# Kernel tuning notes

Hardware: AMD Instinct MI355X
Metric: run time of the kernel (lower is better)

Reference implementation:

```python
import jax, jax.numpy as jnp
import numpy as np

N = 50000      # nodes
E = 800000     # edges (avg degree 16)
F_IN = 64      # node_features (== GENConv out, so no input projection)
H = 64         # hidden
EXP = 2 * H    # GENConv MLP expansion dim = 128
D2 = F_IN + H  # dense-block concat dim = SAGEConv in = 128
EPS_MSG = 1e-7 # GENConv message eps
BN_EPS = 1e-5


def setup_inputs() -> dict:
    key = jax.random.key(0)
    ks = jax.random.split(key, 16)
    g = lambda k, shape, fan: jax.random.normal(k, shape, jnp.float32) / np.sqrt(fan)
    return {
        "x": jax.random.normal(ks[0], (N, F_IN), jnp.float32),
        "edge_index": jax.random.randint(ks[1], (2, E), 0, N, jnp.int32),
        # GENConv MLP: Linear(64,128) -> BatchNorm(128) -> ReLU -> Linear(128,64)
        "W1": g(ks[2], (H, EXP), H), "b1": jnp.zeros((EXP,), jnp.float32),
        "gamma": jnp.ones((EXP,), jnp.float32), "beta": jnp.zeros((EXP,), jnp.float32),
        "W2": g(ks[3], (EXP, H), EXP), "b2": jnp.zeros((H,), jnp.float32),
        # SAGEConv project Linear(128,128), lin_l Linear(128,64), lin_r Linear(128,64,bias=False)
        "Wp": g(ks[4], (D2, D2), D2), "bp": jnp.zeros((D2,), jnp.float32),
        "Wl": g(ks[5], (D2, H), D2), "bl": jnp.zeros((H,), jnp.float32),
        "Wr": g(ks[6], (D2, H), D2),
        # fc Linear(64,1)
        "Wf": g(ks[7], (H, 1), H), "bf": jnp.zeros((1,), jnp.float32),
    }


def _forward(x, W1, b1, gamma, beta, W2, b2, Wp, bp, Wl, bl, Wr, Wf, bf, src, dst):
    n = x.shape[0]
    # ---- GENConv(aggr='softmax', t=1.0): msg = relu(x_j) + eps -------------
    msg = jax.nn.relu(x[src]) + EPS_MSG                       # [E, H]
    mmax = jax.ops.segment_max(msg, dst, num_segments=n)      # per-dst, per-feature max
    mmax = jax.lax.stop_gradient(jnp.where(jnp.isfinite(mmax), mmax, 0.0))
    e = jnp.exp(msg - mmax[dst])                              # t = 1.0
    denom = jax.ops.segment_sum(e, dst, num_segments=n)
    numer = jax.ops.segment_sum(e * msg, dst, num_segments=n)
    agg = numer / jnp.where(denom > 0, denom, 1.0)            # softmax aggregation
    out = agg + x                                             # residual with x_dst
    # GENConv MLP (BatchNorm in training mode: batch stats, biased var)
    h = out @ W1 + b1
    mu = h.mean(axis=0)
    var = h.var(axis=0)
    h = (h - mu) * jax.lax.rsqrt(var + BN_EPS) * gamma + beta
    h = jax.nn.relu(h) @ W2 + b2                              # [N, H]
    # ---- DeepGCNLayer block='dense': concat input ---------------------------
    x2 = jnp.concatenate([x, h], axis=-1)                     # [N, F_IN+H]
    x2 = jax.nn.sigmoid(x2)                                   # self.relu = Sigmoid()
    # ---- SAGEConv(project=True, aggr=DeepSetsAggregation()==sum) -----------
    xp = jax.nn.relu(x2 @ Wp + bp)                            # projected source feats
    aggr = jax.ops.segment_sum(xp[src], dst, num_segments=n)  # DeepSets w/o nns = sum
    out2 = aggr @ Wl + bl + x2 @ Wr                           # root uses UNprojected x2
    out2 = jax.nn.sigmoid(out2)
    logits = out2 @ Wf + bf                                   # [N, 1]
    probs = jax.nn.sigmoid(logits)                            # training branch
    return probs, logits


def reference(x, edge_index, W1, b1, gamma, beta, W2, b2, Wp, bp, Wl, bl, Wr, Wf, bf):
    src, dst = edge_index[0], edge_index[1]
    return _forward(x, W1, b1, gamma, beta, W2, b2, Wp, bp, Wl, bl, Wr, Wf, bf, src, dst)
```

## Files before the change

kernel.cpp:

```cpp
#include <hip/hip_runtime.h>

#define F_IN 64
#define HID 64
#define EXPD 128
#define D2 128
#define MAXDEG 64
#define NBW 128
#define NB 391
#define BINCAP 2400
#define EPT 32

typedef __attribute__((ext_vector_type(8))) short bf16x8;
typedef __attribute__((ext_vector_type(4))) float f32x4;

__device__ __forceinline__ float sigmoidf_(float x) {
    return 1.0f / (1.0f + __expf(-x));
}
__device__ __forceinline__ unsigned bf16rne_(float f) {
    unsigned u = __float_as_uint(f);
    return (u + 0x7FFFu + ((u >> 16) & 1u)) >> 16;
}
__device__ __forceinline__ float bf16tof_(unsigned u16) {
    return __uint_as_float(u16 << 16);
}

__global__ __launch_bounds__(256) void k_bin(const int* __restrict__ ei,
                                             int* __restrict__ binCount,
                                             unsigned* __restrict__ binned,
                                             const float* __restrict__ x,
                                             unsigned short* __restrict__ x16,
                                             const float* __restrict__ W1,
                                             const float* __restrict__ W2,
                                             const float* __restrict__ Wp,
                                             const float* __restrict__ Wl,
                                             const float* __restrict__ Wr,
                                             short* __restrict__ dst,
                                             int nE, int n, int nbinb) {
    int b = blockIdx.x;
    if (b < nbinb) {
        __shared__ int hist[NB];
        __shared__ int base[NB];
        int tid = threadIdx.x;
        for (int i = tid; i < NB; i += 256) hist[i] = 0;
        __syncthreads();
        unsigned ed[EPT];
        unsigned short rk[EPT];
        int e0 = b * (256 * EPT);
#pragma unroll
        for (int j = 0; j < EPT; ++j) {
            int e = e0 + j * 256 + tid;
            if (e < nE) {
                unsigned s = (unsigned)ei[e];
                unsigned d = (unsigned)ei[nE + e];
                ed[j] = s | (d << 16);
                rk[j] = (unsigned short)atomicAdd(&hist[d >> 7], 1);
            }
        }
        __syncthreads();
        for (int i = tid; i < NB; i += 256) {
            int h = hist[i];
            base[i] = h > 0 ? atomicAdd(&binCount[i], h) : 0;
        }
        __syncthreads();
#pragma unroll
        for (int j = 0; j < EPT; ++j) {
            int e = e0 + j * 256 + tid;
            if (e < nE) {
                int bin = (ed[j] >> 16) >> 7;
                int pos = base[bin] + (int)rk[j];
                if (pos < BINCAP) binned[(size_t)bin * BINCAP + pos] = ed[j];
            }
        }
        return;
    }
    b -= nbinb;
    if (b < 192) {
        int e = b * 256 + threadIdx.x;
        const float* src;
        int K, N, base2;
        if (e < 8192)       { src = W1; K = 64;  N = 128; base2 = 0; }
        else if (e < 16384) { src = W2; K = 128; N = 64;  base2 = 8192; }
        else if (e < 32768) { src = Wp; K = 128; N = 128; base2 = 16384; }
        else if (e < 40960) { src = Wl; K = 128; N = 64;  base2 = 32768; }
        else                { src = Wr; K = 128; N = 64;  base2 = 40960; }
        int le = e - base2;
        int j = le & 7;
        int lane = (le >> 3) & 63;
        int n16 = lane & 15, q = lane >> 4;
        int rest = le >> 9;
        int KC = K / 32;
        int kc = rest % KC, nt = rest / KC;
        int k = kc * 32 + q * 8 + j;
        int col = nt * 16 + n16;
        dst[e] = (short)bf16rne_(src[(size_t)k * N + col]);
        return;
    }
    int i0 = (b - 192) * 1024 + threadIdx.x * 4;
    if (i0 < n * F_IN) {
        float4 v = *(const float4*)(x + i0);
        uint2 pk;
        pk.x = bf16rne_(v.x) | (bf16rne_(v.y) << 16);
        pk.y = bf16rne_(v.z) | (bf16rne_(v.w) << 16);
        *(uint2*)(x16 + i0) = pk;
    }
}

__global__ __launch_bounds__(256) void k_csr(const int* __restrict__ binCount,
                                             const unsigned* __restrict__ binned,
                                             int* __restrict__ counts,
                                             unsigned short* __restrict__ csr, int n) {
    __shared__ unsigned short lcsr[NBW * MAXDEG];
    __shared__ int lcnt[NBW];
    int b = blockIdx.x;
    int tid = threadIdx.x;
    if (tid < NBW) lcnt[tid] = 0;
    __syncthreads();
    int cnt = binCount[b];
    cnt = cnt < BINCAP ? cnt : BINCAP;
    const unsigned* src = binned + (size_t)b * BINCAP;
    for (int i = tid; i < cnt; i += 256) {
        unsigned u = src[i];
        int dl = (int)(u >> 16) - b * NBW;
        int slot = atomicAdd(&lcnt[dl], 1);
        if (slot < MAXDEG) lcsr[dl * MAXDEG + slot] = (unsigned short)(u & 0xFFFF);
    }
    __syncthreads();
    int nodebase = b * NBW;
    if (tid < NBW && nodebase + tid < n) counts[nodebase + tid] = lcnt[tid];
    int nrows = n - nodebase;
    nrows = nrows < NBW ? nrows : NBW;
    int nu4 = nrows * 8;
    uint4* dstrow = (uint4*)(csr + (size_t)nodebase * MAXDEG);
    for (int idx = tid; idx < nu4; idx += 256) dstrow[idx] = ((const uint4*)lcsr)[idx];
}

__global__ __launch_bounds__(256) void k_gen(const unsigned short* __restrict__ x16,
                                             const int* __restrict__ counts,
                                             const unsigned short* __restrict__ csr,
                                             unsigned short* __restrict__ gen16, int n) {
    const unsigned* x32 = (const unsigned*)x16;
    int wid = threadIdx.x >> 6;
    int lane = threadIdx.x & 63;
    int H = lane >> 5, f2 = lane & 31;
    int v = blockIdx.x * 4 + wid;
    if (v >= n) return;
    int deg = counts[v];
    deg = deg > MAXDEG ? MAXDEG : deg;
    int idx = 0;
    if (lane < deg) idx = (int)csr[(size_t)v * MAXDEG + lane];
    float d0 = 0.f, d1 = 0.f, n0 = 0.f, n1 = 0.f;
    int i = 0;
    for (; i + 8 <= deg; i += 8) {
        int sA = __shfl(idx, i + 0 + H, 64);
        int sB = __shfl(idx, i + 2 + H, 64);
        int sC = __shfl(idx, i + 4 + H, 64);
        int sD = __shfl(idx, i + 6 + H, 64);
        unsigned uA = x32[(size_t)sA * 32 + f2];
        unsigned uB = x32[(size_t)sB * 32 + f2];
        unsigned uC = x32[(size_t)sC * 32 + f2];
        unsigned uD = x32[(size_t)sD * 32 + f2];
#pragma unroll
        for (int t = 0; t < 4; ++t) {
            unsigned u = t == 0 ? uA : t == 1 ? uB : t == 2 ? uC : uD;
            float m0 = fmaxf(bf16tof_(u & 0xFFFF), 0.f) + 1e-7f;
            float m1 = fmaxf(bf16tof_(u >> 16), 0.f) + 1e-7f;
            float e0 = __expf(m0), e1 = __expf(m1);
            d0 += e0; d1 += e1;
            n0 = fmaf(e0, m0, n0);
            n1 = fmaf(e1, m1, n1);
        }
    }
    for (; i + 2 <= deg; i += 2) {
        int s = __shfl(idx, i + H, 64);
        unsigned u = x32[(size_t)s * 32 + f2];
        float m0 = fmaxf(bf16tof_(u & 0xFFFF), 0.f) + 1e-7f;
        float m1 = fmaxf(bf16tof_(u >> 16), 0.f) + 1e-7f;
        float e0 = __expf(m0), e1 = __expf(m1);
        d0 += e0; d1 += e1;
        n0 = fmaf(e0, m0, n0);
        n1 = fmaf(e1, m1, n1);
    }
    if (i < deg) {
        int s = __shfl(idx, i, 64);
        if (H == 0) {
            unsigned u = x32[(size_t)s * 32 + f2];
            float m0 = fmaxf(bf16tof_(u & 0xFFFF), 0.f) + 1e-7f;
            float m1 = fmaxf(bf16tof_(u >> 16), 0.f) + 1e-7f;
            float e0 = __expf(m0), e1 = __expf(m1);
            d0 += e0; d1 += e1;
            n0 = fmaf(e0, m0, n0);
            n1 = fmaf(e1, m1, n1);
        }
    }
    d0 += __shfl_xor(d0, 32, 64);
    d1 += __shfl_xor(d1, 32, 64);
    n0 += __shfl_xor(n0, 32, 64);
    n1 += __shfl_xor(n1, 32, 64);
    if (H == 0) {
        float a0 = (deg > 0) ? (n0 / d0) : 0.f;
        float a1 = (deg > 0) ? (n1 / d1) : 0.f;
        unsigned xv = x32[(size_t)v * 32 + f2];
        float r0 = a0 + bf16tof_(xv & 0xFFFF);
        float r1 = a1 + bf16tof_(xv >> 16);
        ((unsigned*)gen16)[(size_t)v * 32 + f2] =
            bf16rne_(r0) | (bf16rne_(r1) << 16);
    }
}

__global__ __launch_bounds__(256) void k_gemm1(const unsigned short* __restrict__ gen16,
                                               const short* __restrict__ Wf,
                                               const float* __restrict__ b1,
                                               unsigned short* __restrict__ h16,
                                               float* __restrict__ bnsums, int n) {
    __shared__ short As[64 * 64];
    __shared__ float bnred[256];
    int tid = threadIdx.x;
    int rblk = blockIdx.x * 64;
    if (tid < 256) bnred[tid] = 0.f;
#pragma unroll
    for (int it = 0; it < 2; ++it) {
        int c = it * 256 + tid;
        int rr = c & 63, q8 = c >> 6;
        int gr = rblk + rr;
        gr = gr < n ? gr : n - 1;
        uint4 v = *(const uint4*)(gen16 + (size_t)gr * F_IN + q8 * 8);
        int slot = ((rr >> 4) * 2 + (q8 >> 2)) * 64 + (q8 & 3) * 16 + (rr & 15);
        *(uint4*)(As + slot * 8) = v;
    }
    __syncthreads();
    int L = tid & 63, w = tid >> 6;
    int q = L >> 4, n16 = L & 15;
    int mt_base = (w & 1) * 2;
    int nt_base = (w >> 1) * 4;
    f32x4 acc[2][4];
#pragma unroll
    for (int mt = 0; mt < 2; ++mt)
#pragma unroll
        for (int nt = 0; nt < 4; ++nt) acc[mt][nt] = (f32x4){0.f, 0.f, 0.f, 0.f};
#pragma unroll
    for (int kc = 0; kc < 2; ++kc) {
        bf16x8 a0 = *(const bf16x8*)(As + (((mt_base + 0) * 2 + kc) * 64 + L) * 8);
        bf16x8 a1 = *(const bf16x8*)(As + (((mt_base + 1) * 2 + kc) * 64 + L) * 8);
#pragma unroll
        for (int nt = 0; nt < 4; ++nt) {
            bf16x8 b = *(const bf16x8*)(Wf + (size_t)(((nt_base + nt) * 2 + kc) * 64 + L) * 8);
            acc[0][nt] = __builtin_amdgcn_mfma_f32_16x16x32_bf16(a0, b, acc[0][nt], 0, 0, 0);
            acc[1][nt] = __builtin_amdgcn_mfma_f32_16x16x32_bf16(a1, b, acc[1][nt], 0, 0, 0);
        }
    }
#pragma unroll
    for (int nt = 0; nt < 4; ++nt) {
        int col = (nt_base + nt) * 16 + n16;
        float bv = b1[col];
        float s = 0.f, s2 = 0.f;
#pragma unroll
        for (int mt = 0; mt < 2; ++mt)
#pragma unroll
            for (int r = 0; r < 4; ++r) {
                int row = rblk + (w & 1) * 32 + mt * 16 + q * 4 + r;
                float hv = acc[mt][nt][r] + bv;
                if (row < n) {
                    h16[(size_t)row * EXPD + col] = (unsigned short)bf16rne_(hv);
                    s += hv;
                    s2 = fmaf(hv, hv, s2);
                }
            }
        s += __shfl_xor(s, 16, 64);
        s += __shfl_xor(s, 32, 64);
        s2 += __shfl_xor(s2, 16, 64);
        s2 += __shfl_xor(s2, 32, 64);
        if (q == 0) {
            atomicAdd(&bnred[col], s);
            atomicAdd(&bnred[128 + col], s2);
        }
    }
    __syncthreads();
    if (tid < 256) atomicAdd(&bnsums[tid], bnred[tid]);
}

__global__ __launch_bounds__(256) void k_mlp2a(const unsigned short* __restrict__ h16,
                                               const float* __restrict__ bnsums,
                                               const float* __restrict__ gamma,
                                               const float* __restrict__ beta,
                                               const short* __restrict__ Wf,
                                               const float* __restrict__ b2,
                                               const unsigned short* __restrict__ x16,
                                               unsigned short* __restrict__ x2_16,
                                               float inv_n, int n) {
    __shared__ short As[128 * 128];
    __shared__ float ssl[256];
    int tid = threadIdx.x;
    int rblk = blockIdx.x * 128;
    if (tid < 128) {
        float mu = bnsums[tid] * inv_n;
        float var = fmaf(-mu, mu, bnsums[128 + tid] * inv_n);
        float rs = rsqrtf(fmaxf(var, 0.f) + 1e-5f);
        float scale = gamma[tid] * rs;
        ssl[tid] = scale;
        ssl[128 + tid] = fmaf(-mu, scale, beta[tid]);
    }
    __syncthreads();
#pragma unroll
    for (int it = 0; it < 8; ++it) {
        int c = it * 256 + tid;
        int rr = c & 127, q8 = c >> 7;
        int gr = rblk + rr;
        gr = gr < n ? gr : n - 1;
        uint4 v = *(const uint4*)(h16 + (size_t)gr * EXPD + q8 * 8);
        float4 sc1 = *(const float4*)(ssl + q8 * 8);
        float4 sc2 = *(const float4*)(ssl + q8 * 8 + 4);
        float4 sh1 = *(const float4*)(ssl + 128 + q8 * 8);
        float4 sh2 = *(const float4*)(ssl + 128 + q8 * 8 + 4);
        float o0 = fmaxf(fmaf(bf16tof_(v.x & 0xFFFF), sc1.x, sh1.x), 0.f);
        float o1 = fmaxf(fmaf(bf16tof_(v.x >> 16),    sc1.y, sh1.y), 0.f);
        float o2 = fmaxf(fmaf(bf16tof_(v.y & 0xFFFF), sc1.z, sh1.z), 0.f);
        float o3 = fmaxf(fmaf(bf16tof_(v.y >> 16),    sc1.w, sh1.w), 0.f);
        float o4 = fmaxf(fmaf(bf16tof_(v.z & 0xFFFF), sc2.x, sh2.x), 0.f);
        float o5 = fmaxf(fmaf(bf16tof_(v.z >> 16),    sc2.y, sh2.y), 0.f);
        float o6 = fmaxf(fmaf(bf16tof_(v.w & 0xFFFF), sc2.z, sh2.z), 0.f);
        float o7 = fmaxf(fmaf(bf16tof_(v.w >> 16),    sc2.w, sh2.w), 0.f);
        uint4 pk;
        pk.x = bf16rne_(o0) | (bf16rne_(o1) << 16);
        pk.y = bf16rne_(o2) | (bf16rne_(o3) << 16);
        pk.z = bf16rne_(o4) | (bf16rne_(o5) << 16);
        pk.w = bf16rne_(o6) | (bf16rne_(o7) << 16);
        int slot = ((rr >> 4) * 4 + (q8 >> 2)) * 64 + (q8 & 3) * 16 + (rr & 15);
        *(uint4*)(As + slot * 8) = pk;
    }
    __syncthreads();
    int L = tid & 63, w = tid >> 6;
    int q = L >> 4, n16 = L & 15;
    int mt_base = w * 2;
    f32x4 acc[2][4];
#pragma unroll
    for (int mt = 0; mt < 2; ++mt)
#pragma unroll
        for (int nt = 0; nt < 4; ++nt) acc[mt][nt] = (f32x4){0.f, 0.f, 0.f, 0.f};
#pragma unroll
    for (int kc = 0; kc < 4; ++kc) {
        bf16x8 a0 = *(const bf16x8*)(As + (((mt_base + 0) * 4 + kc) * 64 + L) * 8);
        bf16x8 a1 = *(const bf16x8*)(As + (((mt_base + 1) * 4 + kc) * 64 + L) * 8);
#pragma unroll
        for (int nt = 0; nt < 4; ++nt) {
            bf16x8 b = *(const bf16x8*)(Wf + (size_t)((nt * 4 + kc) * 64 + L) * 8);
            acc[0][nt] = __builtin_amdgcn_mfma_f32_16x16x32_bf16(a0, b, acc[0][nt], 0, 0, 0);
            acc[1][nt] = __builtin_amdgcn_mfma_f32_16x16x32_bf16(a1, b, acc[1][nt], 0, 0, 0);
        }
    }
#pragma unroll
    for (int it = 0; it < 8; ++it) {
        int i = it * 256 + tid;
        int rr = i >> 4, c4 = i & 15;
        int row = rblk + rr;
        if (row < n) {
            uint2 xv = ((const uint2*)x16)[(size_t)row * 16 + c4];
            float s0 = sigmoidf_(bf16tof_(xv.x & 0xFFFF));
            float s1 = sigmoidf_(bf16tof_(xv.x >> 16));
            float s2 = sigmoidf_(bf16tof_(xv.y & 0xFFFF));
            float s3 = sigmoidf_(bf16tof_(xv.y >> 16));
            uint2 pk;
            pk.x = bf16rne_(s0) | (bf16rne_(s1) << 16);
            pk.y = bf16rne_(s2) | (bf16rne_(s3) << 16);
            *(uint2*)(x2_16 + (size_t)row * D2 + c4 * 4) = pk;
        }
    }
#pragma unroll
    for (int nt = 0; nt < 4; ++nt) {
        int col = nt * 16 + n16;
        float bv = b2[col];
#pragma unroll
        for (int mt = 0; mt < 2; ++mt)
#pragma unroll
            for (int r = 0; r < 4; ++r) {
                int row = rblk + w * 32 + mt * 16 + q * 4 + r;
                if (row < n)
                    x2_16[(size_t)row * D2 + 64 + col] =
                        (unsigned short)bf16rne_(sigmoidf_(acc[mt][nt][r] + bv));
            }
    }
}

__global__ __launch_bounds__(256) void k_mlp2b(const unsigned short* __restrict__ x2_16,
                                               const short* __restrict__ Wfp,
                                               const short* __restrict__ Wfl,
                                               const short* __restrict__ Wfr,
                                               const float* __restrict__ bp,
                                               unsigned short* __restrict__ yp16,
                                               unsigned short* __restrict__ yr16, int n) {
    __shared__ short As[64 * 128];
    int tid = threadIdx.x;
    int rblk = blockIdx.x * 64;
#pragma unroll
    for (int it = 0; it < 4; ++it) {
        int c = it * 256 + tid;
        int rr = c & 63, q8 = c >> 6;
        int gr = rblk + rr;
        gr = gr < n ? gr : n - 1;
        uint4 v = *(const uint4*)(x2_16 + (size_t)gr * D2 + q8 * 8);
        int slot = ((rr >> 4) * 4 + (q8 >> 2)) * 64 + (q8 & 3) * 16 + (rr & 15);
        *(uint4*)(As + slot * 8) = v;
    }
    __syncthreads();
    int L = tid & 63, w = tid >> 6;
    int q = L >> 4, n16 = L & 15;
    int mt_base = (w & 1) * 2;
    int nt_base = (w >> 1) * 4;
    f32x4 acc[2][4];
    f32x4 accr[2][2];
#pragma unroll
    for (int mt = 0; mt < 2; ++mt) {
#pragma unroll
        for (int nt = 0; nt < 4; ++nt) acc[mt][nt] = (f32x4){0.f, 0.f, 0.f, 0.f};
#pragma unroll
        for (int nt = 0; nt < 2; ++nt) accr[mt][nt] = (f32x4){0.f, 0.f, 0.f, 0.f};
    }
#pragma unroll
    for (int kc = 0; kc < 4; ++kc) {
        bf16x8 a0 = *(const bf16x8*)(As + (((mt_base + 0) * 4 + kc) * 64 + L) * 8);
        bf16x8 a1 = *(const bf16x8*)(As + (((mt_base + 1) * 4 + kc) * 64 + L) * 8);
#pragma unroll
        for (int nt = 0; nt < 4; ++nt) {
            bf16x8 b = *(const bf16x8*)(Wfp + (size_t)(((nt_base + nt) * 4 + kc) * 64 + L) * 8);
            acc[0][nt] = __builtin_amdgcn_mfma_f32_16x16x32_bf16(a0, b, acc[0][nt], 0, 0, 0);
            acc[1][nt] = __builtin_amdgcn_mfma_f32_16x16x32_bf16(a1, b, acc[1][nt], 0, 0, 0);
        }
#pragma unroll
        for (int nt = 0; nt < 2; ++nt) {
            bf16x8 b = *(const bf16x8*)(Wfr + (size_t)((((w >> 1) * 2 + nt) * 4 + kc) * 64 + L) * 8);
            accr[0][nt] = __builtin_amdgcn_mfma_f32_16x16x32_bf16(a0, b, accr[0][nt], 0, 0, 0);
            accr[1][nt] = __builtin_amdgcn_mfma_f32_16x16x32_bf16(a1, b, accr[1][nt], 0, 0, 0);
        }
    }
#pragma unroll
    for (int nt = 0; nt < 2; ++nt) {
        int col = ((w >> 1) * 2 + nt) * 16 + n16;
#pragma unroll
        for (int mt = 0; mt < 2; ++mt)
#pragma unroll
            for (int r = 0; r < 4; ++r) {
                int row = rblk + (w & 1) * 32 + mt * 16 + q * 4 + r;
                if (row < n)
                    yr16[(size_t)row * HID + col] = (unsigned short)bf16rne_(accr[mt][nt][r]);
            }
    }
    __syncthreads();
#pragma unroll
    for (int nt = 0; nt < 4; ++nt) {
        int kk = (nt_base + nt) * 16 + n16;
        float bv = bp[kk];
        int q8b = kk >> 3, jb = kk & 7;
#pragma unroll
        for (int mt = 0; mt < 2; ++mt)
#pragma unroll
            for (int r = 0; r < 4; ++r) {
                int rr2 = (w & 1) * 32 + mt * 16 + q * 4 + r;
                float xv = fmaxf(acc[mt][nt][r] + bv, 0.f);
                int slot = ((rr2 >> 4) * 4 + (q8b >> 2)) * 64 + (q8b & 3) * 16 + (rr2 & 15);
                As[slot * 8 + jb] = (short)bf16rne_(xv);
            }
    }
    __syncthreads();
    f32x4 acc2[4];
#pragma unroll
    for (int nt = 0; nt < 4; ++nt) acc2[nt] = (f32x4){0.f, 0.f, 0.f, 0.f};
#pragma unroll
    for (int kc = 0; kc < 4; ++kc) {
        bf16x8 a = *(const bf16x8*)(As + ((w * 4 + kc) * 64 + L) * 8);
#pragma unroll
        for (int nt = 0; nt < 4; ++nt) {
            bf16x8 b = *(const bf16x8*)(Wfl + (size_t)((nt * 4 + kc) * 64 + L) * 8);
            acc2[nt] = __builtin_amdgcn_mfma_f32_16x16x32_bf16(a, b, acc2[nt], 0, 0, 0);
        }
    }
#pragma unroll
    for (int nt = 0; nt < 4; ++nt) {
        int col = nt * 16 + n16;
#pragma unroll
        for (int r = 0; r < 4; ++r) {
            int row = rblk + w * 16 + q * 4 + r;
            if (row < n)
                yp16[(size_t)row * HID + col] = (unsigned short)bf16rne_(acc2[nt][r]);
        }
    }
}

__global__ __launch_bounds__(256) void k_sagef(const unsigned short* __restrict__ yp16,
                                               const int* __restrict__ counts,
                                               const unsigned short* __restrict__ csr,
                                               const unsigned short* __restrict__ yr16,
                                               const float* __restrict__ bl,
                                               const float* __restrict__ Wfv,
                                               const float* __restrict__ bf,
                                               float* __restrict__ out, int n) {
    const unsigned* yp32 = (const unsigned*)yp16;
    int wid = threadIdx.x >> 6;
    int lane = threadIdx.x & 63;
    int H = lane >> 5, f2 = lane & 31;
    int v = blockIdx.x * 4 + wid;
    if (v >= n) return;
    int deg = counts[v];
    deg = deg > MAXDEG ? MAXDEG : deg;
    int idx = 0;
    if (lane < deg) idx = (int)csr[(size_t)v * MAXDEG + lane];
    float a0 = 0.f, a1 = 0.f;
    int i = 0;
    for (; i + 8 <= deg; i += 8) {
        int sA = __shfl(idx, i + 0 + H, 64);
        int sB = __shfl(idx, i + 2 + H, 64);
        int sC = __shfl(idx, i + 4 + H, 64);
        int sD = __shfl(idx, i + 6 + H, 64);
        unsigned uA = yp32[(size_t)sA * 32 + f2];
        unsigned uB = yp32[(size_t)sB * 32 + f2];
        unsigned uC = yp32[(size_t)sC * 32 + f2];
        unsigned uD = yp32[(size_t)sD * 32 + f2];
        a0 += bf16tof_(uA & 0xFFFF) + bf16tof_(uB & 0xFFFF) +
              bf16tof_(uC & 0xFFFF) + bf16tof_(uD & 0xFFFF);
        a1 += bf16tof_(uA >> 16) + bf16tof_(uB >> 16) +
              bf16tof_(uC >> 16) + bf16tof_(uD >> 16);
    }
    for (; i + 2 <= deg; i += 2) {
        int s = __shfl(idx, i + H, 64);
        unsigned u = yp32[(size_t)s * 32 + f2];
        a0 += bf16tof_(u & 0xFFFF);
        a1 += bf16tof_(u >> 16);
    }
    if (i < deg) {
        int s = __shfl(idx, i, 64);
        if (H == 0) {
            unsigned u = yp32[(size_t)s * 32 + f2];
            a0 += bf16tof_(u & 0xFFFF);
            a1 += bf16tof_(u >> 16);
        }
    }
    a0 += __shfl_xor(a0, 32, 64);
    a1 += __shfl_xor(a1, 32, 64);
    if (H == 0) {
        unsigned u = ((const unsigned*)yr16)[(size_t)v * 32 + f2];
        float2 blv = ((const float2*)bl)[f2];
        float2 wv  = ((const float2*)Wfv)[f2];
        float o0 = sigmoidf_(a0 + blv.x + bf16tof_(u & 0xFFFF));
        float o1 = sigmoidf_(a1 + blv.y + bf16tof_(u >> 16));
        float t = fmaf(o0, wv.x, o1 * wv.y);
        t += __shfl_xor(t, 1, 64);
        t += __shfl_xor(t, 2, 64);
        t += __shfl_xor(t, 4, 64);
        t += __shfl_xor(t, 8, 64);
        t += __shfl_xor(t, 16, 64);
        if (f2 == 0) {
            float lg = t + bf[0];
            out[v] = sigmoidf_(lg);
            out[n + v] = lg;
        }
    }
}

extern "C" void kernel_launch(void* const* d_in, const int* in_sizes, int n_in,
                              void* d_out, int out_size, void* d_ws, size_t ws_size,
                              hipStream_t stream) {
    const float* x     = (const float*)d_in[0];
    const int*   ei    = (const int*)d_in[1];
    const float* W1    = (const float*)d_in[2];
    const float* b1    = (const float*)d_in[3];
    const float* gamma = (const float*)d_in[4];
    const float* beta  = (const float*)d_in[5];
    const float* W2    = (const float*)d_in[6];
    const float* b2    = (const float*)d_in[7];
    const float* Wp    = (const float*)d_in[8];
    const float* bp    = (const float*)d_in[9];
    const float* Wl    = (const float*)d_in[10];
    const float* bl    = (const float*)d_in[11];
    const float* Wr    = (const float*)d_in[12];
    const float* Wfv   = (const float*)d_in[13];
    const float* bf    = (const float*)d_in[14];
    const int n = in_sizes[0] / F_IN;
    const int e = in_sizes[1] / 2;

    char* ws = (char*)d_ws;
    size_t off = 0;
    auto alloc = [&](size_t bytes) -> void* {
        void* p = (void*)(ws + off);
        off += (bytes + 255) & ~(size_t)255;
        return p;
    };
    float*          bnsums   = (float*)alloc(256 * 4 + NB * 4);
    int*            binCount = (int*)((char*)bnsums + 1024);
    int*            counts   = (int*)alloc((size_t)n * 4);
    unsigned short* csr      = (unsigned short*)alloc((size_t)n * MAXDEG * 2);
    unsigned*       binned   = (unsigned*)alloc((size_t)NB * BINCAP * 4);
    unsigned short* x16      = (unsigned short*)alloc((size_t)n * F_IN * 2);
    unsigned short* gen16    = (unsigned short*)alloc((size_t)n * F_IN * 2);
    unsigned short* h16      = (unsigned short*)alloc((size_t)n * EXPD * 2);
    unsigned short* x2_16    = (unsigned short*)alloc((size_t)n * D2 * 2);
    unsigned short* yp16     = (unsigned short*)alloc((size_t)n * HID * 2);
    unsigned short* yr16     = (unsigned short*)alloc((size_t)n * HID * 2);
    short*          wfrag    = (short*)alloc(49152 * 2);

    float* out = (float*)d_out;
    const int nb64  = (n + 63) / 64;
    const int nb128 = (n + 127) / 128;
    const int nb4   = (n + 3) / 4;
    const int nbinb = (e + 256 * EPT - 1) / (256 * EPT);
    const int nfp = nbinb + 192 + ((n * F_IN + 1023) / 1024);

    hipMemsetAsync(bnsums, 0, 1024 + NB * 4, stream);

    k_bin<<<nfp, 256, 0, stream>>>(ei, binCount, binned, x, x16, W1, W2, Wp, Wl,
                                   Wr, wfrag, e, n, nbinb);
    k_csr<<<NB, 256, 0, stream>>>(binCount, binned, counts, csr, n);
    k_gen<<<nb4, 256, 0, stream>>>(x16, counts, csr, gen16, n);
    k_gemm1<<<nb64, 256, 0, stream>>>(gen16, wfrag, b1, h16, bnsums, n);
    k_mlp2a<<<nb128, 256, 0, stream>>>(h16, bnsums, gamma, beta, wfrag + 8192, b2,
                                       x16, x2_16, 1.0f / (float)n, n);
    k_mlp2b<<<nb64, 256, 0, stream>>>(x2_16, wfrag + 16384, wfrag + 32768,
                                      wfrag + 40960, bp, yp16, yr16, n);
    k_sagef<<<nb4, 256, 0, stream>>>(yp16, counts, csr, yr16, bl, Wfv, bf, out, n);
}
```

Before: 228.9 us.

## Fuse softmax aggregation into GEMM1, merge MLP kernels, drop global bin atomics

The GENConv softmax gather now runs inside the first GEMM kernel and writes its result straight to shared memory, so the gen16 intermediate disappears. The two MLP kernels are merged so the x2 concat/sigmoid tile stays on-chip instead of passing through global memory. Edge binning now uses per-block sub-bins with fixed capacity instead of global atomics, and the memset is folded into k_bin. Costs: 64-row blocks with serial per-wave gathers give fewer waves for latency hiding, and a per-block sub-bin cap of 64 could drop edges on skewed inputs.

```diff
diff --git a/kernel.cpp b/kernel.cpp
--- a/kernel.cpp
+++ b/kernel.cpp
@@ -7,7 +7,8 @@
 #define MAXDEG 64
 #define NBW 128
 #define NB 391
-#define BINCAP 2400
+#define NBINB 98
+#define SUBCAP 64
 #define EPT 32
 
 typedef __attribute__((ext_vector_type(8))) short bf16x8;
@@ -25,8 +26,8 @@
 }
 
 __global__ __launch_bounds__(256) void k_bin(const int* __restrict__ ei,
-                                             int* __restrict__ binCount,
-                                             unsigned* __restrict__ binned,
+                                             int* __restrict__ cnt2,
+                                             unsigned* __restrict__ binned2,
                                              const float* __restrict__ x,
                                              unsigned short* __restrict__ x16,
                                              const float* __restrict__ W1,
@@ -35,12 +36,13 @@
                                              const float* __restrict__ Wl,
                                              const float* __restrict__ Wr,
                                              short* __restrict__ dst,
+                                             float* __restrict__ bnsums,
                                              int nE, int n, int nbinb) {
     int b = blockIdx.x;
+    int tid = threadIdx.x;
     if (b < nbinb) {
         __shared__ int hist[NB];
-        __shared__ int base[NB];
-        int tid = threadIdx.x;
+        if (b == 0) bnsums[tid] = 0.f;
         for (int i = tid; i < NB; i += 256) hist[i] = 0;
         __syncthreads();
         unsigned ed[EPT];
@@ -57,25 +59,22 @@
             }
         }
         __syncthreads();
-        for (int i = tid; i < NB; i += 256) {
-            int h = hist[i];
-            base[i] = h > 0 ? atomicAdd(&binCount[i], h) : 0;
-        }
-        __syncthreads();
+        for (int i = tid; i < NB; i += 256) cnt2[b * NB + i] = hist[i];
 #pragma unroll
         for (int j = 0; j < EPT; ++j) {
             int e = e0 + j * 256 + tid;
             if (e < nE) {
                 int bin = (ed[j] >> 16) >> 7;
-                int pos = base[bin] + (int)rk[j];
-                if (pos < BINCAP) binned[(size_t)bin * BINCAP + pos] = ed[j];
+                int r = (int)rk[j];
+                if (r < SUBCAP)
+                    binned2[((size_t)bin * nbinb + b) * SUBCAP + r] = ed[j];
             }
         }
         return;
     }
     b -= nbinb;
     if (b < 192) {
-        int e = b * 256 + threadIdx.x;
+        int e = b * 256 + tid;
         const float* src;
         int K, N, base2;
         if (e < 8192)       { src = W1; K = 64;  N = 128; base2 = 0; }
@@ -95,7 +94,7 @@
         dst[e] = (short)bf16rne_(src[(size_t)k * N + col]);
         return;
     }
-    int i0 = (b - 192) * 1024 + threadIdx.x * 4;
+    int i0 = (b - 192) * 1024 + tid * 4;
     if (i0 < n * F_IN) {
         float4 v = *(const float4*)(x + i0);
         uint2 pk;
@@ -105,24 +104,33 @@
     }
 }
 
-__global__ __launch_bounds__(256) void k_csr(const int* __restrict__ binCount,
-                                             const unsigned* __restrict__ binned,
+__global__ __launch_bounds__(256) void k_csr(const int* __restrict__ cnt2,
+                                             const unsigned* __restrict__ binned2,
                                              int* __restrict__ counts,
-                                             unsigned short* __restrict__ csr, int n) {
+                                             unsigned short* __restrict__ csr,
+                                             int n, int nbinb) {
     __shared__ unsigned short lcsr[NBW * MAXDEG];
     __shared__ int lcnt[NBW];
+    __shared__ int scnt[NBINB];
     int b = blockIdx.x;
     int tid = threadIdx.x;
     if (tid < NBW) lcnt[tid] = 0;
-    __syncthreads();
-    int cnt = binCount[b];
-    cnt = cnt < BINCAP ? cnt : BINCAP;
-    const unsigned* src = binned + (size_t)b * BINCAP;
-    for (int i = tid; i < cnt; i += 256) {
-        unsigned u = src[i];
-        int dl = (int)(u >> 16) - b * NBW;
-        int slot = atomicAdd(&lcnt[dl], 1);
-        if (slot < MAXDEG) lcsr[dl * MAXDEG + slot] = (unsigned short)(u & 0xFFFF);
+    for (int i = tid; i < nbinb; i += 256) {
+        int c = cnt2[i * NB + b];
+        scnt[i] = c < SUBCAP ? c : SUBCAP;
+    }
+    __syncthreads();
+    const unsigned* src = binned2 + (size_t)b * nbinb * SUBCAP;
+    int tot = nbinb * SUBCAP;
+    for (int i = tid; i < tot; i += 256) {
+        int blk = i >> 6;
+        int r = i & (SUBCAP - 1);
+        if (r < scnt[blk]) {
+            unsigned u = src[i];
+            int dl = (int)(u >> 16) - b * NBW;
+            int slot = atomicAdd(&lcnt[dl], 1);
+            if (slot < MAXDEG) lcsr[dl * MAXDEG + slot] = (unsigned short)(u & 0xFFFF);
+        }
     }
     __syncthreads();
     int nodebase = b * NBW;
@@ -134,101 +142,95 @@
     for (int idx = tid; idx < nu4; idx += 256) dstrow[idx] = ((const uint4*)lcsr)[idx];
 }
 
-__global__ __launch_bounds__(256) void k_gen(const unsigned short* __restrict__ x16,
-                                             const int* __restrict__ counts,
-                                             const unsigned short* __restrict__ csr,
-                                             unsigned short* __restrict__ gen16, int n) {
-    const unsigned* x32 = (const unsigned*)x16;
-    int wid = threadIdx.x >> 6;
-    int lane = threadIdx.x & 63;
-    int H = lane >> 5, f2 = lane & 31;
-    int v = blockIdx.x * 4 + wid;
-    if (v >= n) return;
-    int deg = counts[v];
-    deg = deg > MAXDEG ? MAXDEG : deg;
-    int idx = 0;
-    if (lane < deg) idx = (int)csr[(size_t)v * MAXDEG + lane];
-    float d0 = 0.f, d1 = 0.f, n0 = 0.f, n1 = 0.f;
-    int i = 0;
-    for (; i + 8 <= deg; i += 8) {
-        int sA = __shfl(idx, i + 0 + H, 64);
-        int sB = __shfl(idx, i + 2 + H, 64);
-        int sC = __shfl(idx, i + 4 + H, 64);
-        int sD = __shfl(idx, i + 6 + H, 64);
-        unsigned uA = x32[(size_t)sA * 32 + f2];
-        unsigned uB = x32[(size_t)sB * 32 + f2];
-        unsigned uC = x32[(size_t)sC * 32 + f2];
-        unsigned uD = x32[(size_t)sD * 32 + f2];
-#pragma unroll
-        for (int t = 0; t < 4; ++t) {
-            unsigned u = t == 0 ? uA : t == 1 ? uB : t == 2 ? uC : uD;
-            float m0 = fmaxf(bf16tof_(u & 0xFFFF), 0.f) + 1e-7f;
-            float m1 = fmaxf(bf16tof_(u >> 16), 0.f) + 1e-7f;
-            float e0 = __expf(m0), e1 = __expf(m1);
-            d0 += e0; d1 += e1;
-            n0 = fmaf(e0, m0, n0);
-            n1 = fmaf(e1, m1, n1);
-        }
-    }
-    for (; i + 2 <= deg; i += 2) {
-        int s = __shfl(idx, i + H, 64);
-        unsigned u = x32[(size_t)s * 32 + f2];
-        float m0 = fmaxf(bf16tof_(u & 0xFFFF), 0.f) + 1e-7f;
-        float m1 = fmaxf(bf16tof_(u >> 16), 0.f) + 1e-7f;
-        float e0 = __expf(m0), e1 = __expf(m1);
-        d0 += e0; d1 += e1;
-        n0 = fmaf(e0, m0, n0);
-        n1 = fmaf(e1, m1, n1);
-    }
-    if (i < deg) {
-        int s = __shfl(idx, i, 64);
-        if (H == 0) {
-            unsigned u = x32[(size_t)s * 32 + f2];
-            float m0 = fmaxf(bf16tof_(u & 0xFFFF), 0.f) + 1e-7f;
-            float m1 = fmaxf(bf16tof_(u >> 16), 0.f) + 1e-7f;
-            float e0 = __expf(m0), e1 = __expf(m1);
-            d0 += e0; d1 += e1;
-            n0 = fmaf(e0, m0, n0);
-            n1 = fmaf(e1, m1, n1);
-        }
-    }
-    d0 += __shfl_xor(d0, 32, 64);
-    d1 += __shfl_xor(d1, 32, 64);
-    n0 += __shfl_xor(n0, 32, 64);
-    n1 += __shfl_xor(n1, 32, 64);
-    if (H == 0) {
-        float a0 = (deg > 0) ? (n0 / d0) : 0.f;
-        float a1 = (deg > 0) ? (n1 / d1) : 0.f;
-        unsigned xv = x32[(size_t)v * 32 + f2];
-        float r0 = a0 + bf16tof_(xv & 0xFFFF);
-        float r1 = a1 + bf16tof_(xv >> 16);
-        ((unsigned*)gen16)[(size_t)v * 32 + f2] =
-            bf16rne_(r0) | (bf16rne_(r1) << 16);
-    }
-}
-
-__global__ __launch_bounds__(256) void k_gemm1(const unsigned short* __restrict__ gen16,
-                                               const short* __restrict__ Wf,
-                                               const float* __restrict__ b1,
-                                               unsigned short* __restrict__ h16,
-                                               float* __restrict__ bnsums, int n) {
+__global__ __launch_bounds__(256) void k_geng(const unsigned short* __restrict__ x16,
+                                              const int* __restrict__ counts,
+                                              const unsigned short* __restrict__ csr,
+                                              const short* __restrict__ Wf,
+                                              const float* __restrict__ b1,
+                                              unsigned short* __restrict__ h16,
+                                              float* __restrict__ bnsums, int n) {
     __shared__ short As[64 * 64];
     __shared__ float bnred[256];
+    const unsigned* x32 = (const unsigned*)x16;
     int tid = threadIdx.x;
+    int w = tid >> 6;
+    int lane = tid & 63;
+    int H = lane >> 5, f2 = lane & 31;
     int rblk = blockIdx.x * 64;
-    if (tid < 256) bnred[tid] = 0.f;
-#pragma unroll
-    for (int it = 0; it < 2; ++it) {
-        int c = it * 256 + tid;
-        int rr = c & 63, q8 = c >> 6;
-        int gr = rblk + rr;
-        gr = gr < n ? gr : n - 1;
-        uint4 v = *(const uint4*)(gen16 + (size_t)gr * F_IN + q8 * 8);
+    bnred[tid] = 0.f;
+    for (int t = 0; t < 16; ++t) {
+        int rr = w * 16 + t;
+        int v = rblk + rr;
+        int q8 = f2 >> 2;
         int slot = ((rr >> 4) * 2 + (q8 >> 2)) * 64 + (q8 & 3) * 16 + (rr & 15);
-        *(uint4*)(As + slot * 8) = v;
-    }
-    __syncthreads();
-    int L = tid & 63, w = tid >> 6;
+        if (v < n) {
+            int deg = counts[v];
+            deg = deg > MAXDEG ? MAXDEG : deg;
+            int idx = 0;
+            if (lane < deg) idx = (int)csr[(size_t)v * MAXDEG + lane];
+            float d0 = 0.f, d1 = 0.f, n0 = 0.f, n1 = 0.f;
+            int i = 0;
+            for (; i + 8 <= deg; i += 8) {
+                int sA = __shfl(idx, i + 0 + H, 64);
+                int sB = __shfl(idx, i + 2 + H, 64);
+                int sC = __shfl(idx, i + 4 + H, 64);
+                int sD = __shfl(idx, i + 6 + H, 64);
+                unsigned uA = x32[(size_t)sA * 32 + f2];
+                unsigned uB = x32[(size_t)sB * 32 + f2];
+                unsigned uC = x32[(size_t)sC * 32 + f2];
+                unsigned uD = x32[(size_t)sD * 32 + f2];
+#pragma unroll
+                for (int tt = 0; tt < 4; ++tt) {
+                    unsigned u = tt == 0 ? uA : tt == 1 ? uB : tt == 2 ? uC : uD;
+                    float m0 = fmaxf(bf16tof_(u & 0xFFFF), 0.f) + 1e-7f;
+                    float m1 = fmaxf(bf16tof_(u >> 16), 0.f) + 1e-7f;
+                    float e0 = __expf(m0), e1 = __expf(m1);
+                    d0 += e0; d1 += e1;
+                    n0 = fmaf(e0, m0, n0);
+                    n1 = fmaf(e1, m1, n1);
+                }
+            }
+            for (; i + 2 <= deg; i += 2) {
+                int s = __shfl(idx, i + H, 64);
+                unsigned u = x32[(size_t)s * 32 + f2];
+                float m0 = fmaxf(bf16tof_(u & 0xFFFF), 0.f) + 1e-7f;
+                float m1 = fmaxf(bf16tof_(u >> 16), 0.f) + 1e-7f;
+                float e0 = __expf(m0), e1 = __expf(m1);
+                d0 += e0; d1 += e1;
+                n0 = fmaf(e0, m0, n0);
+                n1 = fmaf(e1, m1, n1);
+            }
+            if (i < deg) {
+                int s = __shfl(idx, i, 64);
+                if (H == 0) {
+                    unsigned u = x32[(size_t)s * 32 + f2];
+                    float m0 = fmaxf(bf16tof_(u & 0xFFFF), 0.f) + 1e-7f;
+                    float m1 = fmaxf(bf16tof_(u >> 16), 0.f) + 1e-7f;
+                    float e0 = __expf(m0), e1 = __expf(m1);
+                    d0 += e0; d1 += e1;
+                    n0 = fmaf(e0, m0, n0);
+                    n1 = fmaf(e1, m1, n1);
+                }
+            }
+            d0 += __shfl_xor(d0, 32, 64);
+            d1 += __shfl_xor(d1, 32, 64);
+            n0 += __shfl_xor(n0, 32, 64);
+            n1 += __shfl_xor(n1, 32, 64);
+            if (H == 0) {
+                float a0 = (deg > 0) ? (n0 / d0) : 0.f;
+                float a1 = (deg > 0) ? (n1 / d1) : 0.f;
+                unsigned xv = x32[(size_t)v * 32 + f2];
+                float r0 = a0 + bf16tof_(xv & 0xFFFF);
+                float r1 = a1 + bf16tof_(xv >> 16);
+                *(unsigned*)(As + slot * 8 + (f2 & 3) * 2) =
+                    bf16rne_(r0) | (bf16rne_(r1) << 16);
+            }
+        } else {
+            if (H == 0) *(unsigned*)(As + slot * 8 + (f2 & 3) * 2) = 0u;
+        }
+    }
+    __syncthreads();
+    int L = lane;
     int q = L >> 4, n16 = L & 15;
     int mt_base = (w & 1) * 2;
     int nt_base = (w >> 1) * 4;
@@ -275,22 +277,28 @@
         }
     }
     __syncthreads();
-    if (tid < 256) atomicAdd(&bnsums[tid], bnred[tid]);
-}
-
-__global__ __launch_bounds__(256) void k_mlp2a(const unsigned short* __restrict__ h16,
-                                               const float* __restrict__ bnsums,
-                                               const float* __restrict__ gamma,
-                                               const float* __restrict__ beta,
-                                               const short* __restrict__ Wf,
-                                               const float* __restrict__ b2,
-                                               const unsigned short* __restrict__ x16,
-                                               unsigned short* __restrict__ x2_16,
-                                               float inv_n, int n) {
-    __shared__ short As[128 * 128];
+    atomicAdd(&bnsums[tid], bnred[tid]);
+}
+
+__global__ __launch_bounds__(256) void k_mlp2ab(const unsigned short* __restrict__ h16,
+                                                const float* __restrict__ bnsums,
+                                                const float* __restrict__ gamma,
+                                                const float* __restrict__ beta,
+                                                const short* __restrict__ Wf2,
+                                                const float* __restrict__ b2,
+                                                const unsigned short* __restrict__ x16,
+                                                const short* __restrict__ Wfp,
+                                                const short* __restrict__ Wfl,
+                                                const short* __restrict__ Wfr,
+                                                const float* __restrict__ bp,
+                                                unsigned short* __restrict__ yp16,
+                                                unsigned short* __restrict__ yr16,
+                                                float inv_n, int n) {
+    __shared__ short Bs[64 * 128];
+    __shared__ short As[64 * 128];
     __shared__ float ssl[256];
     int tid = threadIdx.x;
-    int rblk = blockIdx.x * 128;
+    int rblk = blockIdx.x * 64;
     if (tid < 128) {
         float mu = bnsums[tid] * inv_n;
         float var = fmaf(-mu, mu, bnsums[128 + tid] * inv_n);
@@ -301,9 +309,9 @@
     }
     __syncthreads();
 #pragma unroll
-    for (int it = 0; it < 8; ++it) {
+    for (int it = 0; it < 4; ++it) {
         int c = it * 256 + tid;
-        int rr = c & 127, q8 = c >> 7;
+        int rr = c & 63, q8 = c >> 6;
         int gr = rblk + rr;
         gr = gr < n ? gr : n - 1;
         uint4 v = *(const uint4*)(h16 + (size_t)gr * EXPD + q8 * 8);
@@ -325,84 +333,69 @@
         pk.z = bf16rne_(o4) | (bf16rne_(o5) << 16);
         pk.w = bf16rne_(o6) | (bf16rne_(o7) << 16);
         int slot = ((rr >> 4) * 4 + (q8 >> 2)) * 64 + (q8 & 3) * 16 + (rr & 15);
-        *(uint4*)(As + slot * 8) = pk;
-    }
-    __syncthreads();
-    int L = tid & 63, w = tid >> 6;
-    int q = L >> 4, n16 = L & 15;
-    int mt_base = w * 2;
-    f32x4 acc[2][4];
-#pragma unroll
-    for (int mt = 0; mt < 2; ++mt)
-#pragma unroll
-        for (int nt = 0; nt < 4; ++nt) acc[mt][nt] = (f32x4){0.f, 0.f, 0.f, 0.f};
-#pragma unroll
-    for (int kc = 0; kc < 4; ++kc) {
-        bf16x8 a0 = *(const bf16x8*)(As + (((mt_base + 0) * 4 + kc) * 64 + L) * 8);
-        bf16x8 a1 = *(const bf16x8*)(As + (((mt_base + 1) * 4 + kc) * 64 + L) * 8);
-#pragma unroll
-        for (int nt = 0; nt < 4; ++nt) {
-            bf16x8 b = *(const bf16x8*)(Wf + (size_t)((nt * 4 + kc) * 64 + L) * 8);
-            acc[0][nt] = __builtin_amdgcn_mfma_f32_16x16x32_bf16(a0, b, acc[0][nt], 0, 0, 0);
-            acc[1][nt] = __builtin_amdgcn_mfma_f32_16x16x32_bf16(a1, b, acc[1][nt], 0, 0, 0);
-        }
-    }
-#pragma unroll
-    for (int it = 0; it < 8; ++it) {
-        int i = it * 256 + tid;
-        int rr = i >> 4, c4 = i & 15;
-        int row = rblk + rr;
-        if (row < n) {
-            uint2 xv = ((const uint2*)x16)[(size_t)row * 16 + c4];
-            float s0 = sigmoidf_(bf16tof_(xv.x & 0xFFFF));
-            float s1 = sigmoidf_(bf16tof_(xv.x >> 16));
-            float s2 = sigmoidf_(bf16tof_(xv.y & 0xFFFF));
-            float s3 = sigmoidf_(bf16tof_(xv.y >> 16));
-            uint2 pk;
-            pk.x = bf16rne_(s0) | (bf16rne_(s1) << 16);
-            pk.y = bf16rne_(s2) | (bf16rne_(s3) << 16);
-            *(uint2*)(x2_16 + (size_t)row * D2 + c4 * 4) = pk;
-        }
-    }
-#pragma unroll
-    for (int nt = 0; nt < 4; ++nt) {
-        int col = nt * 16 + n16;
-        float bv = b2[col];
-#pragma unroll
-        for (int mt = 0; mt < 2; ++mt)
-#pragma unroll
-            for (int r = 0; r < 4; ++r) {
-                int row = rblk + w * 32 + mt * 16 + q * 4 + r;
-                if (row < n)
-                    x2_16[(size_t)row * D2 + 64 + col] =
-                        (unsigned short)bf16rne_(sigmoidf_(acc[mt][nt][r] + bv));
-            }
-    }
-}
-
-__global__ __launch_bounds__(256) void k_mlp2b(const unsigned short* __restrict__ x2_16,
-                                               const short* __restrict__ Wfp,
-                                               const short* __restrict__ Wfl,
-                                               const short* __restrict__ Wfr,
-                                               const float* __restrict__ bp,
-                                               unsigned short* __restrict__ yp16,
-                                               unsigned short* __restrict__ yr16, int n) {
-    __shared__ short As[64 * 128];
-    int tid = threadIdx.x;
-    int rblk = blockIdx.x * 64;
-#pragma unroll
-    for (int it = 0; it < 4; ++it) {
+        *(uint4*)(Bs + slot * 8) = pk;
+    }
+#pragma unroll
+    for (int it = 0; it < 2; ++it) {
         int c = it * 256 + tid;
         int rr = c & 63, q8 = c >> 6;
         int gr = rblk + rr;
         gr = gr < n ? gr : n - 1;
-        uint4 v = *(const uint4*)(x2_16 + (size_t)gr * D2 + q8 * 8);
+        uint4 v = *(const uint4*)(x16 + (size_t)gr * F_IN + q8 * 8);
+        float o0 = sigmoidf_(bf16tof_(v.x & 0xFFFF));
+        float o1 = sigmoidf_(bf16tof_(v.x >> 16));
+        float o2 = sigmoidf_(bf16tof_(v.y & 0xFFFF));
+        float o3 = sigmoidf_(bf16tof_(v.y >> 16));
+        float o4 = sigmoidf_(bf16tof_(v.z & 0xFFFF));
+        float o5 = sigmoidf_(bf16tof_(v.z >> 16));
+        float o6 = sigmoidf_(bf16tof_(v.w & 0xFFFF));
+        float o7 = sigmoidf_(bf16tof_(v.w >> 16));
+        uint4 pk;
+        pk.x = bf16rne_(o0) | (bf16rne_(o1) << 16);
+        pk.y = bf16rne_(o2) | (bf16rne_(o3) << 16);
+        pk.z = bf16rne_(o4) | (bf16rne_(o5) << 16);
+        pk.w = bf16rne_(o6) | (bf16rne_(o7) << 16);
         int slot = ((rr >> 4) * 4 + (q8 >> 2)) * 64 + (q8 & 3) * 16 + (rr & 15);
-        *(uint4*)(As + slot * 8) = v;
+        *(uint4*)(As + slot * 8) = pk;
     }
     __syncthreads();
     int L = tid & 63, w = tid >> 6;
     int q = L >> 4, n16 = L & 15;
+    {
+        int mtb = (w & 1) * 2, ntb = (w >> 1) * 2;
+        f32x4 acch[2][2];
+#pragma unroll
+        for (int mt = 0; mt < 2; ++mt)
+#pragma unroll
+            for (int nt = 0; nt < 2; ++nt) acch[mt][nt] = (f32x4){0.f, 0.f, 0.f, 0.f};
+#pragma unroll
+        for (int kc = 0; kc < 4; ++kc) {
+            bf16x8 a0 = *(const bf16x8*)(Bs + (((mtb + 0) * 4 + kc) * 64 + L) * 8);
+            bf16x8 a1 = *(const bf16x8*)(Bs + (((mtb + 1) * 4 + kc) * 64 + L) * 8);
+#pragma unroll
+            for (int nt = 0; nt < 2; ++nt) {
+                bf16x8 b = *(const bf16x8*)(Wf2 + (size_t)(((ntb + nt) * 4 + kc) * 64 + L) * 8);
+                acch[0][nt] = __builtin_amdgcn_mfma_f32_16x16x32_bf16(a0, b, acch[0][nt], 0, 0, 0);
+                acch[1][nt] = __builtin_amdgcn_mfma_f32_16x16x32_bf16(a1, b, acch[1][nt], 0, 0, 0);
+            }
+        }
+#pragma unroll
+        for (int nt = 0; nt < 2; ++nt) {
+            int col = (ntb + nt) * 16 + n16;
+            float bv = b2[col];
+            int q8b = 8 + (col >> 3), jb = col & 7;
+#pragma unroll
+            for (int mt = 0; mt < 2; ++mt)
+#pragma unroll
+                for (int r = 0; r < 4; ++r) {
+                    int rr2 = (w & 1) * 32 + mt * 16 + q * 4 + r;
+                    float hv = sigmoidf_(acch[mt][nt][r] + bv);
+                    int slot = ((rr2 >> 4) * 4 + (q8b >> 2)) * 64 + (q8b & 3) * 16 + (rr2 & 15);
+                    As[slot * 8 + jb] = (short)bf16rne_(hv);
+                }
+        }
+    }
+    __syncthreads();
     int mt_base = (w & 1) * 2;
     int nt_base = (w >> 1) * 4;
     f32x4 acc[2][4];
@@ -443,7 +436,6 @@
                     yr16[(size_t)row * HID + col] = (unsigned short)bf16rne_(accr[mt][nt][r]);
             }
     }
-    __syncthreads();
 #pragma unroll
     for (int nt = 0; nt < 4; ++nt) {
         int kk = (nt_base + nt) * 16 + n16;
@@ -456,7 +448,7 @@
                 int rr2 = (w & 1) * 32 + mt * 16 + q * 4 + r;
                 float xv = fmaxf(acc[mt][nt][r] + bv, 0.f);
                 int slot = ((rr2 >> 4) * 4 + (q8b >> 2)) * 64 + (q8b & 3) * 16 + (rr2 & 15);
-                As[slot * 8 + jb] = (short)bf16rne_(xv);
+                Bs[slot * 8 + jb] = (short)bf16rne_(xv);
             }
     }
     __syncthreads();
@@ -465,7 +457,7 @@
     for (int nt = 0; nt < 4; ++nt) acc2[nt] = (f32x4){0.f, 0.f, 0.f, 0.f};
 #pragma unroll
     for (int kc = 0; kc < 4; ++kc) {
-        bf16x8 a = *(const bf16x8*)(As + ((w * 4 + kc) * 64 + L) * 8);
+        bf16x8 a = *(const bf16x8*)(Bs + ((w * 4 + kc) * 64 + L) * 8);
 #pragma unroll
         for (int nt = 0; nt < 4; ++nt) {
             bf16x8 b = *(const bf16x8*)(Wfl + (size_t)((nt * 4 + kc) * 64 + L) * 8);
@@ -582,36 +574,30 @@
         off += (bytes + 255) & ~(size_t)255;
         return p;
     };
-    float*          bnsums   = (float*)alloc(256 * 4 + NB * 4);
-    int*            binCount = (int*)((char*)bnsums + 1024);
+    const int nbinb = (e + 256 * EPT - 1) / (256 * EPT);
+    float*          bnsums   = (float*)alloc(256 * 4);
+    int*            cnt2     = (int*)alloc((size_t)nbinb * NB * 4);
     int*            counts   = (int*)alloc((size_t)n * 4);
     unsigned short* csr      = (unsigned short*)alloc((size_t)n * MAXDEG * 2);
-    unsigned*       binned   = (unsigned*)alloc((size_t)NB * BINCAP * 4);
+    unsigned*       binned2  = (unsigned*)alloc((size_t)NB * nbinb * SUBCAP * 4);
     unsigned short* x16      = (unsigned short*)alloc((size_t)n * F_IN * 2);
-    unsigned short* gen16    = (unsigned short*)alloc((size_t)n * F_IN * 2);
     unsigned short* h16      = (unsigned short*)alloc((size_t)n * EXPD * 2);
-    unsigned short* x2_16    = (unsigned short*)alloc((size_t)n * D2 * 2);
     unsigned short* yp16     = (unsigned short*)alloc((size_t)n * HID * 2);
     unsigned short* yr16     = (unsigned short*)alloc((size_t)n * HID * 2);
     short*          wfrag    = (short*)alloc(49152 * 2);
 
     float* out = (float*)d_out;
     const int nb64  = (n + 63) / 64;
-    const int nb128 = (n + 127) / 128;
     const int nb4   = (n + 3) / 4;
-    const int nbinb = (e + 256 * EPT - 1) / (256 * EPT);
     const int nfp = nbinb + 192 + ((n * F_IN + 1023) / 1024);
 
-    hipMemsetAsync(bnsums, 0, 1024 + NB * 4, stream);
-
-    k_bin<<<nfp, 256, 0, stream>>>(ei, binCount, binned, x, x16, W1, W2, Wp, Wl,
-                                   Wr, wfrag, e, n, nbinb);
-    k_csr<<<NB, 256, 0, stream>>>(binCount, binned, counts, csr, n);
-    k_gen<<<nb4, 256, 0, stream>>>(x16, counts, csr, gen16, n);
-    k_gemm1<<<nb64, 256, 0, stream>>>(gen16, wfrag, b1, h16, bnsums, n);
-    k_mlp2a<<<nb128, 256, 0, stream>>>(h16, bnsums, gamma, beta, wfrag + 8192, b2,
-                                       x16, x2_16, 1.0f / (float)n, n);
-    k_mlp2b<<<nb64, 256, 0, stream>>>(x2_16, wfrag + 16384, wfrag + 32768,
-                                      wfrag + 40960, bp, yp16, yr16, n);
+    k_bin<<<nfp, 256, 0, stream>>>(ei, cnt2, binned2, x, x16, W1, W2, Wp, Wl,
+                                   Wr, wfrag, bnsums, e, n, nbinb);
+    k_csr<<<NB, 256, 0, stream>>>(cnt2, binned2, counts, csr, n, nbinb);
+    k_geng<<<nb64, 256, 0, stream>>>(x16, counts, csr, wfrag, b1, h16, bnsums, n);
+    k_mlp2ab<<<nb64, 256, 0, stream>>>(h16, bnsums, gamma, beta, wfrag + 8192, b2,
+                                       x16, wfrag + 16384, wfrag + 32768,
+                                       wfrag + 40960, bp, yp16, yr16,
+                                       1.0f / (float)n, n);
     k_sagef<<<nb4, 256, 0, stream>>>(yp16, counts, csr, yr16, bl, Wfv, bf, out, n);
 }
```

New measurement: 229.6 us. Within noise of the previous version (+0.3%).
